# Kernel optimization log

Hardware: AMD Instinct MI355X
Metric: run time of the kernel (lower is better)

## Reference

```python
import math
import jax, jax.numpy as jnp
import numpy as np

D_MODEL = 512
H = 8          # head_num
HD = 64        # head_dim
ETA = 4
R = 8
D_FFC = 2048
EPS = 1e-6
GRU_BIAS = 2.0
T, B = 128, 32
TOTAL_PROJ = H * HD * 5 + H * ETA * 3  # 2656


def _layer_norm(x, g, b):
    m = x.mean(-1, keepdims=True)
    v = ((x - m) ** 2).mean(-1, keepdims=True)
    return (x - m) / jnp.sqrt(v + 1e-5) * g + b


def _outer(a, b):
    # a: (T,B,H,D), b: (T,B,H,E) -> (T,B,H,D*E), row-major over (D,E) like torch bmm+reshape
    t, bb, h, d = a.shape
    return (a[..., :, None] * b[..., None, :]).reshape(t, bb, h, d * b.shape[-1])


def _gru_gate(x, y, w, u):
    # GTrXL-style gating: x = residual stream, y = new signal. w,u: (3, d, d)
    r = jax.nn.sigmoid(y @ w[0].T + x @ u[0].T)
    z = jax.nn.sigmoid(y @ w[1].T + x @ u[1].T - GRU_BIAS)
    h = jnp.tanh(y @ w[2].T + (r * x) @ u[2].T)
    return (1.0 - z) * x + z * h


def _discounted_sum(prev, x, d):
    # y_t = d_t * y_{t-1} + x_t, y_{-1} = prev. x: (T, ...), d broadcastable to x.
    def step(c, xd):
        xi, di = xd
        nc = di * c + xi
        return nc, nc
    _, ys = jax.lax.scan(step, prev, (x, d))
    return ys


def setup_inputs() -> dict:
    key = jax.random.key(0)
    ks = jax.random.split(key, 12)
    sc_p = 1.0 / math.sqrt(D_MODEL)
    return {
        "inputs": jax.random.normal(ks[0], (T, B, D_MODEL), jnp.float32),
        "terminations": jax.random.randint(ks[1], (T, B), 0, 2).astype(jnp.int32),
        "tilde_k": jnp.zeros((B, R, H, ETA * HD), jnp.float32),
        "tilde_v": jnp.zeros((B, R, H, HD), jnp.float32),
        "s_prev": jnp.zeros((B, H, ETA * HD), jnp.float32),
        "tick": jnp.zeros((B, 1), jnp.float32),
        "w_proj": jax.random.normal(ks[2], (TOTAL_PROJ, D_MODEL), jnp.float32) * sc_p,
        "b_proj": jnp.zeros((TOTAL_PROJ,), jnp.float32),
        "w_attn": jax.random.normal(ks[3], (D_MODEL, H * HD), jnp.float32) * (1.0 / math.sqrt(H * HD)),
        "b_attn": jnp.zeros((D_MODEL,), jnp.float32),
        "ln1_g": jnp.ones((D_MODEL,), jnp.float32),
        "ln1_b": jnp.zeros((D_MODEL,), jnp.float32),
        "ln2_g": jnp.ones((D_MODEL,), jnp.float32),
        "ln2_b": jnp.zeros((D_MODEL,), jnp.float32),
        "gru1_w": jax.random.normal(ks[4], (3, D_MODEL, D_MODEL), jnp.float32) * sc_p,
        "gru1_u": jax.random.normal(ks[5], (3, D_MODEL, D_MODEL), jnp.float32) * sc_p,
        "gru2_w": jax.random.normal(ks[6], (3, D_MODEL, D_MODEL), jnp.float32) * sc_p,
        "gru2_u": jax.random.normal(ks[7], (3, D_MODEL, D_MODEL), jnp.float32) * sc_p,
        "ffc_w1": jax.random.normal(ks[8], (D_FFC, D_MODEL), jnp.float32) * sc_p,
        "ffc_b1": jnp.zeros((D_FFC,), jnp.float32),
        "ffc_w2": jax.random.normal(ks[9], (D_MODEL, D_FFC), jnp.float32) * (1.0 / math.sqrt(D_FFC)),
        "ffc_b2": jnp.zeros((D_MODEL,), jnp.float32),
    }


def _forward(inputs, terminations, tilde_k, tilde_v, s_prev, tick,
             w_proj, b_proj, w_attn, b_attn, ln1_g, ln1_b, ln2_g, ln2_b,
             gru1_w, gru1_u, gru2_w, gru2_u, ffc_w1, ffc_b1, ffc_w2, ffc_b2):
    t, bsz, _ = inputs.shape
    omegas = jnp.linspace(-math.pi, math.pi, R).astype(inputs.dtype)

    x_normed = _layer_norm(inputs, ln1_g, ln1_b)
    all_proj = x_normed @ w_proj.T + b_proj  # (T,B,2656)
    kqv_dim = H * HD * 5
    kqvbg = all_proj[..., :kqv_dim].reshape(t, bsz, H, 5, HD)
    p123 = all_proj[..., kqv_dim:].reshape(t, bsz, H, 3, ETA)

    keys = kqvbg[..., 0, :]
    queries = kqvbg[..., 1, :]
    values = kqvbg[..., 2, :]
    beta = jax.nn.sigmoid(kqvbg[..., 3, :])
    gammas = kqvbg[..., 4, :]
    p1, p2, p3 = p123[..., 0, :], p123[..., 1, :], p123[..., 2, :]

    keys_exp = _outer(jax.nn.relu(keys), jax.nn.relu(p1))          # (T,B,H,HD*ETA)
    queries_exp = _outer(jax.nn.relu(queries), jax.nn.relu(p2))
    gammas_exp = _outer(jax.nn.sigmoid(gammas), jax.nn.sigmoid(p3))

    ticks = tick[None] + jnp.arange(1, t + 1, dtype=tick.dtype).reshape(t, 1, 1)  # (T,B,1)
    occil = jnp.cos(ticks * omegas)  # (T,B,R)

    values_gated = values * beta                 # (T,B,H,HD)
    keys_gated = keys_exp * gammas_exp           # (T,B,H,HD*ETA)
    s_in = keys_gated
    values_osc = values_gated[:, :, None] * occil[..., None, None]  # (T,B,R,H,HD)
    keys_osc = keys_gated[:, :, None] * occil[..., None, None]      # (T,B,R,H,HD*ETA)

    term_mask = (1.0 - terminations.astype(inputs.dtype))[:, :, None, None]  # (T,B,1,1)
    discount_gamma = (1.0 - gammas_exp) * term_mask   # (T,B,H,HD*ETA)
    discount_beta = (1.0 - beta) * term_mask          # (T,B,H,HD)

    final_keys = _discounted_sum(tilde_k, keys_osc, discount_gamma[:, :, None])
    final_values = _discounted_sum(tilde_v, values_osc, discount_beta[:, :, None])
    final_s = _discounted_sum(s_prev, s_in, discount_gamma)

    kdq = (final_keys * queries_exp[:, :, None]).sum(-1)   # (T,B,R,H)
    kv = (final_values * kdq[..., None]).sum(2)             # (T,B,H,HD)
    norm = (final_s * queries_exp).sum(-1) + EPS            # (T,B,H)
    attn = kv / (2 * R * norm[..., None])
    attn = attn.reshape(t, bsz, H * HD) @ w_attn.T + b_attn  # (T,B,d_model)

    gating1 = _gru_gate(inputs, jax.nn.relu(attn), gru1_w, gru1_u)
    ffc_in = _layer_norm(gating1, ln2_g, ln2_b)
    ffc_out = jax.nn.relu(jax.nn.relu(ffc_in @ ffc_w1.T + ffc_b1) @ ffc_w2.T + ffc_b2)
    output = _gru_gate(gating1, ffc_out, gru2_w, gru2_u)
    return output


def reference(inputs, terminations, tilde_k, tilde_v, s_prev, tick,
              w_proj, b_proj, w_attn, b_attn, ln1_g, ln1_b, ln2_g, ln2_b,
              gru1_w, gru1_u, gru2_w, gru2_u, ffc_w1, ffc_b1, ffc_w2, ffc_b2):
    return _forward(inputs, terminations, tilde_k, tilde_v, s_prev, tick,
                    w_proj, b_proj, w_attn, b_attn, ln1_g, ln1_b, ln2_g, ln2_b,
                    gru1_w, gru1_u, gru2_w, gru2_u, ffc_w1, ffc_b1, ffc_w2, ffc_b2)
```

## Files before the change

kernel.cpp:

```cpp
#include <hip/hip_runtime.h>
#include <hip/hip_bf16.h>
#include <math.h>

#define DM   512
#define HH   8
#define RR   8
#define TT   128
#define BBATCH 32
#define MM   (TT*BBATCH)
#define NPROJ 2656
#define KQV  2560

typedef __attribute__((ext_vector_type(8))) short bf16x8;
typedef __attribute__((ext_vector_type(4))) float f32x4;

__device__ __forceinline__ float sigmoidf_(float x) {
    return 1.0f / (1.0f + __expf(-x));
}

__device__ __forceinline__ void gload_lds16(const void* g, void* l) {
    __builtin_amdgcn_global_load_lds(
        (const __attribute__((address_space(1))) unsigned int*)g,
        (__attribute__((address_space(3))) unsigned int*)l, 16, 0, 0);
}

template<int CTRL, int RMASK>
__device__ __forceinline__ float dpp_add_(float x) {
    union { float f; int i; } a, b;
    a.f = x;
    b.i = __builtin_amdgcn_update_dpp(0, a.i, CTRL, RMASK, 0xf, true);
    return x + b.f;
}
__device__ __forceinline__ float wave_sum_u(float x) {
    x = dpp_add_<0x111, 0xf>(x);
    x = dpp_add_<0x112, 0xf>(x);
    x = dpp_add_<0x114, 0xf>(x);
    x = dpp_add_<0x118, 0xf>(x);
    x = dpp_add_<0x142, 0xa>(x);
    x = dpp_add_<0x143, 0xc>(x);
    union { float f; int i; } s, t;
    s.f = x;
    t.i = __builtin_amdgcn_readlane(s.i, 63);
    return t.f;
}

struct F2B9 {
    const float* s[9];
    __hip_bfloat16* d[9];
    int cum[10];
};

__global__ __launch_bounds__(256) void f2b_ln_all(F2B9 a,
    const float* __restrict__ x, const float* __restrict__ g,
    const float* __restrict__ b, __hip_bfloat16* __restrict__ lnout)
{
    if (blockIdx.x < 8752) {
        int q = blockIdx.x * 256 + threadIdx.x;
        if (q >= a.cum[9]) return;
        int s = 0;
        #pragma unroll
        for (int i = 1; i < 9; ++i) s += (q >= a.cum[i]);
        int i4 = (q - a.cum[s]) * 4;
        float4 v = *(const float4*)(a.s[s] + i4);
        __hip_bfloat16* dst = a.d[s] + i4;
        dst[0] = __float2bfloat16(v.x);
        dst[1] = __float2bfloat16(v.y);
        dst[2] = __float2bfloat16(v.z);
        dst[3] = __float2bfloat16(v.w);
        return;
    }
    int row = blockIdx.x - 8752;
    int tid = threadIdx.x;
    const float* xr = x + (size_t)row * DM;
    float2 v = ((const float2*)xr)[tid];
    float s = v.x + v.y;
    #pragma unroll
    for (int off = 32; off; off >>= 1) s += __shfl_down(s, off);
    __shared__ float red[8];
    int wid = tid >> 6, lane = tid & 63;
    if (lane == 0) red[wid] = s;
    __syncthreads();
    if (tid == 0) red[0] = (red[0] + red[1] + red[2] + red[3]) * (1.0f / DM);
    __syncthreads();
    float mean = red[0];
    float dx = v.x - mean, dy = v.y - mean;
    float sq = dx*dx + dy*dy;
    #pragma unroll
    for (int off = 32; off; off >>= 1) sq += __shfl_down(sq, off);
    if (lane == 0) red[4 + wid] = sq;
    __syncthreads();
    if (tid == 0) red[1] = rsqrtf((red[4]+red[5]+red[6]+red[7]) * (1.0f/DM) + 1e-5f);
    __syncthreads();
    float rstd = red[1];
    float2 gg = ((const float2*)g)[tid];
    float2 bb = ((const float2*)b)[tid];
    __hip_bfloat16* orow = lnout + (size_t)row * DM;
    orow[2*tid+0] = __float2bfloat16(dx * rstd * gg.x + bb.x);
    orow[2*tid+1] = __float2bfloat16(dy * rstd * gg.y + bb.y);
}

__global__ __launch_bounds__(256) void ln_kernel(const float* __restrict__ x,
    const float* __restrict__ g, const float* __restrict__ b,
    __hip_bfloat16* __restrict__ out)
{
    int row = blockIdx.x;
    int tid = threadIdx.x;
    const float* xr = x + (size_t)row * DM;
    float2 v = ((const float2*)xr)[tid];
    float s = v.x + v.y;
    #pragma unroll
    for (int off = 32; off; off >>= 1) s += __shfl_down(s, off);
    __shared__ float red[8];
    int wid = tid >> 6, lane = tid & 63;
    if (lane == 0) red[wid] = s;
    __syncthreads();
    if (tid == 0) red[0] = (red[0] + red[1] + red[2] + red[3]) * (1.0f / DM);
    __syncthreads();
    float mean = red[0];
    float dx = v.x - mean, dy = v.y - mean;
    float sq = dx*dx + dy*dy;
    #pragma unroll
    for (int off = 32; off; off >>= 1) sq += __shfl_down(sq, off);
    if (lane == 0) red[4 + wid] = sq;
    __syncthreads();
    if (tid == 0) red[1] = rsqrtf((red[4]+red[5]+red[6]+red[7]) * (1.0f/DM) + 1e-5f);
    __syncthreads();
    float rstd = red[1];
    float2 gg = ((const float2*)g)[tid];
    float2 bb = ((const float2*)b)[tid];
    __hip_bfloat16* orow = out + (size_t)row * DM;
    orow[2*tid+0] = __float2bfloat16(dx * rstd * gg.x + bb.x);
    orow[2*tid+1] = __float2bfloat16(dy * rstd * gg.y + bb.y);
}

__device__ __forceinline__ void gemm_core128(
    const __hip_bfloat16* __restrict__ A, const __hip_bfloat16* __restrict__ W,
    const float* __restrict__ bias,
    float* __restrict__ Cf, __hip_bfloat16* __restrict__ Cb,
    int N, int K, int act, int m0, int n0,
    __hip_bfloat16* As, __hip_bfloat16* Bs)
{
    int tid = threadIdx.x;
    int wave = tid >> 6, lane = tid & 63;
    int wm = (wave >> 1) * 64, wn = (wave & 1) * 64;
    int fr = lane & 15, fq = lane >> 4;

    f32x4 acc[4][4];
    #pragma unroll
    for (int i = 0; i < 4; ++i)
        #pragma unroll
        for (int j = 0; j < 4; ++j)
            acc[i][j] = (f32x4){0.f, 0.f, 0.f, 0.f};

    int sm0 = wave*16 + fr;
    int sm1 = sm0 + 64;
    int wr0 = n0 + sm0; if (wr0 >= N) wr0 = N - 1;
    int wr1 = n0 + sm1; if (wr1 >= N) wr1 = N - 1;
    const __hip_bfloat16* Ag0 = A + (size_t)(m0 + sm0) * K + fq*8;
    const __hip_bfloat16* Ag1 = A + (size_t)(m0 + sm1) * K + fq*8;
    const __hip_bfloat16* Wg0 = W + (size_t)wr0 * K + fq*8;
    const __hip_bfloat16* Wg1 = W + (size_t)wr1 * K + fq*8;

    for (int k0 = 0; k0 < K; k0 += 32) {
        gload_lds16(Ag0 + k0, As + (size_t)wave*512);
        gload_lds16(Ag1 + k0, As + (size_t)(wave+4)*512);
        gload_lds16(Wg0 + k0, Bs + (size_t)wave*512);
        gload_lds16(Wg1 + k0, Bs + (size_t)(wave+4)*512);
        __syncthreads();
        bf16x8 af[4], bfr[4];
        #pragma unroll
        for (int i = 0; i < 4; ++i) {
            af[i]  = *(const bf16x8*)(As + (size_t)(wm/16 + i)*512 + lane*8);
            bfr[i] = *(const bf16x8*)(Bs + (size_t)(wn/16 + i)*512 + lane*8);
        }
        #pragma unroll
        for (int mi = 0; mi < 4; ++mi)
            #pragma unroll
            for (int ni = 0; ni < 4; ++ni)
                acc[mi][ni] = __builtin_amdgcn_mfma_f32_16x16x32_bf16(
                    af[mi], bfr[ni], acc[mi][ni], 0, 0, 0);
        __syncthreads();
    }

    #pragma unroll
    for (int ni = 0; ni < 4; ++ni) {
        int n = n0 + wn + ni*16 + fr;
        bool nok = n < N;
        float bv = (bias && nok) ? bias[n] : 0.f;
        #pragma unroll
        for (int mi = 0; mi < 4; ++mi) {
            #pragma unroll
            for (int r = 0; r < 4; ++r) {
                int m = m0 + wm + mi*16 + fq*4 + r;
                float v = acc[mi][ni][r] + bv;
                if (act) v = fmaxf(v, 0.f);
                if (nok) {
                    size_t idx = (size_t)m * N + n;
                    if (Cf) Cf[idx] = v;
                    if (Cb) Cb[idx] = __float2bfloat16(v);
                }
            }
        }
    }
}

__global__ __launch_bounds__(256) void gemm_bf16(
    const __hip_bfloat16* __restrict__ A, const __hip_bfloat16* __restrict__ W,
    const float* __restrict__ bias,
    float* __restrict__ Cf, __hip_bfloat16* __restrict__ Cb,
    int N, int K, int act)
{
    __shared__ __attribute__((aligned(16))) __hip_bfloat16 As[8*512];
    __shared__ __attribute__((aligned(16))) __hip_bfloat16 Bs[8*512];
    gemm_core128(A, W, bias, Cf, Cb, N, K, act, blockIdx.y * 128, blockIdx.x * 128, As, Bs);
}

__global__ __launch_bounds__(256) void ffc1_bx_dual(
    const __hip_bfloat16* __restrict__ Aa, const __hip_bfloat16* __restrict__ Wa,
    const float* __restrict__ biasA, __hip_bfloat16* __restrict__ CbA,
    int Na, int splitX,
    const __hip_bfloat16* __restrict__ Ab, const __hip_bfloat16* __restrict__ Wb,
    float* __restrict__ CfB, int Nb, int K)
{
    __shared__ __attribute__((aligned(16))) __hip_bfloat16 As[8*512];
    __shared__ __attribute__((aligned(16))) __hip_bfloat16 Bs[8*512];
    int bx = blockIdx.x;
    if (bx < splitX)
        gemm_core128(Aa, Wa, biasA, nullptr, CbA, Na, K, 1, blockIdx.y*128, bx*128, As, Bs);
    else
        gemm_core128(Ab, Wb, nullptr, CfB, nullptr, Nb, K, 0, blockIdx.y*128, (bx-splitX)*128, As, Bs);
}

__global__ __launch_bounds__(256) void gemm_bf16_64(
    const __hip_bfloat16* __restrict__ A, const __hip_bfloat16* __restrict__ W,
    const float* __restrict__ bias,
    float* __restrict__ Cf, __hip_bfloat16* __restrict__ Cb,
    int N, int K, int act)
{
    __shared__ __attribute__((aligned(16))) __hip_bfloat16 As[4*512];
    __shared__ __attribute__((aligned(16))) __hip_bfloat16 Bs[8*512];
    int tid = threadIdx.x;
    int wave = tid >> 6, lane = tid & 63;
    int m0 = blockIdx.y * 64, n0 = blockIdx.x * 128;
    int wm = (wave >> 1) * 32, wn = (wave & 1) * 64;
    int fr = lane & 15, fq = lane >> 4;

    f32x4 acc[2][4];
    #pragma unroll
    for (int i = 0; i < 2; ++i)
        #pragma unroll
        for (int j = 0; j < 4; ++j)
            acc[i][j] = (f32x4){0.f, 0.f, 0.f, 0.f};

    const __hip_bfloat16* Ag = A + (size_t)(m0 + wave*16 + fr) * K + fq*8;
    int wr0 = n0 + wave*16 + fr; if (wr0 >= N) wr0 = N - 1;
    int wr1 = wr0 + 64;          if (wr1 >= N) wr1 = N - 1;
    const __hip_bfloat16* Wg0 = W + (size_t)wr0 * K + fq*8;
    const __hip_bfloat16* Wg1 = W + (size_t)wr1 * K + fq*8;

    for (int k0 = 0; k0 < K; k0 += 32) {
        gload_lds16(Ag  + k0, As + (size_t)wave*512);
        gload_lds16(Wg0 + k0, Bs + (size_t)wave*512);
        gload_lds16(Wg1 + k0, Bs + (size_t)(wave+4)*512);
        __syncthreads();
        bf16x8 af[2], bfr[4];
        #pragma unroll
        for (int i = 0; i < 2; ++i)
            af[i]  = *(const bf16x8*)(As + (size_t)(wm/16 + i)*512 + lane*8);
        #pragma unroll
        for (int j = 0; j < 4; ++j)
            bfr[j] = *(const bf16x8*)(Bs + (size_t)(wn/16 + j)*512 + lane*8);
        #pragma unroll
        for (int mi = 0; mi < 2; ++mi)
            #pragma unroll
            for (int ni = 0; ni < 4; ++ni)
                acc[mi][ni] = __builtin_amdgcn_mfma_f32_16x16x32_bf16(
                    af[mi], bfr[ni], acc[mi][ni], 0, 0, 0);
        __syncthreads();
    }

    #pragma unroll
    for (int ni = 0; ni < 4; ++ni) {
        int n = n0 + wn + ni*16 + fr;
        bool nok = n < N;
        float bv = (bias && nok) ? bias[n] : 0.f;
        #pragma unroll
        for (int mi = 0; mi < 2; ++mi) {
            #pragma unroll
            for (int r = 0; r < 4; ++r) {
                int m = m0 + wm + mi*16 + fq*4 + r;
                float v = acc[mi][ni][r] + bv;
                if (act) v = fmaxf(v, 0.f);
                if (nok) {
                    size_t idx = (size_t)m * N + n;
                    if (Cf) Cf[idx] = v;
                    if (Cb) Cb[idx] = __float2bfloat16(v);
                }
            }
        }
    }
}

#define NSLOT 16
#define SLOTF 912
#define RSLOT 8
#define RSLOTF 336

__global__ __launch_bounds__(256) void scan_attn_fused(
    const float* __restrict__ proj, const int* __restrict__ term,
    const float* __restrict__ tick, const float* __restrict__ tilde_k,
    const float* __restrict__ tilde_v, const float* __restrict__ s_prev,
    __hip_bfloat16* __restrict__ attn,
    const __hip_bfloat16* __restrict__ gA, const __hip_bfloat16* __restrict__ gW,
    float* __restrict__ gC)
{
    extern __shared__ __attribute__((aligned(16))) char smem_dyn[];
    int bid = blockIdx.x;
    if (bid >= 256) {
        __hip_bfloat16* As = (__hip_bfloat16*)smem_dyn;
        __hip_bfloat16* Bs = As + 8*512;
        int g = bid - 256;
        gemm_core128(gA, gW, nullptr, gC, nullptr, 1024, DM, 0,
                     (g >> 3) * 128, (g & 7) * 128, As, Bs);
        return;
    }

    float* slots    = (float*)smem_dyn;
    float* raw      = slots + NSLOT*SLOTF;
    int*   raw_flag = (int*)(raw + RSLOT*RSLOTF);
    int*   ctrs     = raw_flag + 32;

    const int b = bid >> 3;
    const int h = bid & 7;
    const int tid = threadIdx.x;
    const int wv = tid >> 6, lane = tid & 63;

    if (tid == 0) { ctrs[0] = 0; ctrs[1] = 0; }
    if (tid < 32) raw_flag[tid] = 0;
    __syncthreads();
    int* prod_ctr = &ctrs[0];
    int* cons_ctr = &ctrs[1];

    const float PI_ = 3.14159265358979323846f;

    if (wv >= 2) {
        for (int g = wv - 2; g < TT/4; g += 2) {
            int t0 = g * 4;
            if (t0 >= RSLOT) {
                while (__hip_atomic_load(prod_ctr, __ATOMIC_ACQUIRE,
                                         __HIP_MEMORY_SCOPE_WORKGROUP) < t0 - 4)
                    __builtin_amdgcn_s_sleep(1);
            }
            float va[4][5]; float pv[4];
            #pragma unroll
            for (int i = 0; i < 4; ++i) {
                const float* prow = proj + (size_t)((t0+i)*BBATCH + b) * NPROJ;
                const float* p5 = prow + h*320;
                va[i][0] = p5[lane];
                va[i][1] = p5[64  + lane];
                va[i][2] = p5[128 + lane];
                va[i][3] = p5[192 + lane];
                va[i][4] = p5[256 + lane];
                pv[i] = (lane < 12) ? prow[KQV + h*12 + lane] : 0.f;
            }
            #pragma unroll
            for (int i = 0; i < 4; ++i) {
                float* rs = raw + (size_t)((t0+i) & (RSLOT-1)) * RSLOTF;
                rs[lane]       = va[i][0];
                rs[64  + lane] = va[i][1];
                rs[128 + lane] = va[i][2];
                rs[192 + lane] = va[i][3];
                rs[256 + lane] = va[i][4];
                if (lane < 12) rs[320 + lane] = pv[i];
            }
            if (lane == 0)
                __hip_atomic_store(&raw_flag[g], 1, __ATOMIC_RELEASE,
                                   __HIP_MEMORY_SCOPE_WORKGROUP);
        }
        return;
    }

    if (wv == 1) {
        float tk = tick[b];
        int ta  = term[lane*BBATCH + b];
        int tb_ = term[(64 + lane)*BBATCH + b];
        float wv_ = -PI_ + (float)(lane & 7) * (2.0f * PI_ / 7.0f);
        float cwv = cosf(wv_), swv = sinf(wv_);
        float ocv = cosf((tk + 1.0f) * wv_), osv = sinf((tk + 1.0f) * wv_);

        for (int t0 = 0; t0 < TT; t0 += 4) {
            if (t0 >= NSLOT) {
                while (__hip_atomic_load(cons_ctr, __ATOMIC_ACQUIRE,
                                         __HIP_MEMORY_SCOPE_WORKGROUP) < t0 - (NSLOT - 4))
                    __builtin_amdgcn_s_sleep(1);
            }
            int g = t0 >> 2;
            while (__hip_atomic_load(&raw_flag[g], __ATOMIC_ACQUIRE,
                                     __HIP_MEMORY_SCOPE_WORKGROUP) == 0)
                __builtin_amdgcn_s_sleep(1);
            float va[4][5]; float4 P1[4], P2[4], P3[4];
            #pragma unroll
            for (int i = 0; i < 4; ++i) {
                const float* rs = raw + (size_t)((t0+i) & (RSLOT-1)) * RSLOTF;
                va[i][0] = rs[lane];
                va[i][1] = rs[64  + lane];
                va[i][2] = rs[128 + lane];
                va[i][3] = rs[192 + lane];
                va[i][4] = rs[256 + lane];
                P1[i] = *(const float4*)(rs + 320);
                P2[i] = *(const float4*)(rs + 324);
                P3[i] = *(const float4*)(rs + 328);
            }
            #pragma unroll
            for (int i = 0; i < 4; ++i) {
                int t = t0 + i;
                int tm = (t < 64) ? __builtin_amdgcn_readlane(ta, t)
                                  : __builtin_amdgcn_readlane(tb_, t - 64);
                float mask = 1.0f - (float)tm;
                float kr = fmaxf(va[i][0], 0.f);
                float qr = fmaxf(va[i][1], 0.f);
                float sg = sigmoidf_(va[i][4]);
                float sb = sigmoidf_(va[i][3]);
                float vg = va[i][2] * sb;
                float db = (1.f - sb) * mask;
                float p1a[4] = {P1[i].x, P1[i].y, P1[i].z, P1[i].w};
                float p2a[4] = {P2[i].x, P2[i].y, P2[i].z, P2[i].w};
                float p3a[4] = {P3[i].x, P3[i].y, P3[i].z, P3[i].w};
                float4 qe, kgv, dgv;
                #pragma unroll
                for (int j = 0; j < 4; ++j) {
                    float kexp = kr * fmaxf(p1a[j], 0.f);
                    float qq   = qr * fmaxf(p2a[j], 0.f);
                    float gexp = sg * sigmoidf_(p3a[j]);
                    float kg_  = kexp * gexp;
                    float dg_  = (1.f - gexp) * mask;
                    if (j == 0) { qe.x = qq; kgv.x = kg_; dgv.x = dg_; }
                    if (j == 1) { qe.y = qq; kgv.y = kg_; dgv.y = dg_; }
                    if (j == 2) { qe.z = qq; kgv.z = kg_; dgv.z = dg_; }
                    if (j == 3) { qe.w = qq; kgv.w = kg_; dgv.w = dg_; }
                }
                float* sl = slots + (size_t)(t & (NSLOT-1)) * SLOTF;
                *(float4*)(sl + 4*lane)       = qe;
                *(float4*)(sl + 256 + 4*lane) = kgv;
                *(float4*)(sl + 512 + 4*lane) = dgv;
                sl[768 + lane] = vg;
                sl[832 + lane] = db;
                if (lane < 8) sl[896 + lane] = ocv;
                float cc = ocv, ss = osv;
                ocv = cc*cwv - ss*swv;
                osv = ss*cwv + cc*swv;
            }
            if (lane == 0)
                __hip_atomic_store(prod_ctr, t0 + 4, __ATOMIC_RELEASE,
                                   __HIP_MEMORY_SCOPE_WORKGROUP);
        }
        return;
    }

    float4 fs = *(const float4*)(s_prev + ((size_t)(b*HH + h))*256 + lane*4);
    float4 fk[8];
    #pragma unroll
    for (int r = 0; r < 8; ++r)
        fk[r] = *(const float4*)(tilde_k + (((size_t)b*RR + r)*HH + h)*256 + lane*4);
    float fv[8];
    #pragma unroll
    for (int r = 0; r < 8; ++r)
        fv[r] = tilde_v[(((size_t)b*RR + r)*HH + h)*64 + lane];

    struct PF { float4 qe, kg, dg, o0, o1; float vg, db; };
    auto loadPF = [&](int t, PF& p) {
        if (t < TT) {
            const float* sl = slots + (size_t)(t & (NSLOT-1)) * SLOTF;
            p.qe = *(const float4*)(sl + 4*lane);
            p.kg = *(const float4*)(sl + 256 + 4*lane);
            p.dg = *(const float4*)(sl + 512 + 4*lane);
            p.vg = sl[768 + lane];
            p.db = sl[832 + lane];
            p.o0 = *(const float4*)(sl + 896);
            p.o1 = *(const float4*)(sl + 900);
        }
    };

    auto step = [&](int t, PF c) {
        float qexp[4] = {c.qe.x, c.qe.y, c.qe.z, c.qe.w};
        float kg[4]   = {c.kg.x, c.kg.y, c.kg.z, c.kg.w};
        float dg[4]   = {c.dg.x, c.dg.y, c.dg.z, c.dg.w};
        float occ[8]  = {c.o0.x, c.o0.y, c.o0.z, c.o0.w,
                         c.o1.x, c.o1.y, c.o1.z, c.o1.w};
        fs.x = dg[0]*fs.x + kg[0];
        fs.y = dg[1]*fs.y + kg[1];
        fs.z = dg[2]*fs.z + kg[2];
        fs.w = dg[3]*fs.w + kg[3];
        float snorm = fs.x*qexp[0] + fs.y*qexp[1] + fs.z*qexp[2] + fs.w*qexp[3];
        float kdq[8];
        #pragma unroll
        for (int r = 0; r < 8; ++r) {
            float4 f = fk[r];
            float o = occ[r];
            f.x = dg[0]*f.x + kg[0]*o;
            f.y = dg[1]*f.y + kg[1]*o;
            f.z = dg[2]*f.z + kg[2]*o;
            f.w = dg[3]*f.w + kg[3]*o;
            fk[r] = f;
            kdq[r] = f.x*qexp[0] + f.y*qexp[1] + f.z*qexp[2] + f.w*qexp[3];
        }
        #pragma unroll
        for (int r = 0; r < 8; ++r)
            fv[r] = c.db * fv[r] + c.vg * occ[r];
        float nrm_u = wave_sum_u(snorm);
        float kdq_u[8];
        #pragma unroll
        for (int r = 0; r < 8; ++r)
            kdq_u[r] = wave_sum_u(kdq[r]);
        float kv = 0.f;
        #pragma unroll
        for (int r = 0; r < 8; ++r)
            kv += fv[r] * kdq_u[r];
        attn[(size_t)(t*BBATCH + b)*DM + h*64 + lane] =
            __float2bfloat16(kv / (16.f * (nrm_u + 1e-6f)));
    };

    while (__hip_atomic_load(prod_ctr, __ATOMIC_ACQUIRE,
                             __HIP_MEMORY_SCOPE_WORKGROUP) < 8)
        __builtin_amdgcn_s_sleep(1);
    PF pf0, pf1;
    loadPF(0, pf0);
    loadPF(1, pf1);

    for (int t = 0; t < TT; t += 2) {
        if ((t & 3) == 0) {
            if ((t & 7) == 0 && t >= 8 && lane == 0)
                __hip_atomic_store(cons_ctr, t - 2, __ATOMIC_RELEASE,
                                   __HIP_MEMORY_SCOPE_WORKGROUP);
            int tgt = (t + 8 > TT) ? TT : t + 8;
            while (__hip_atomic_load(prod_ctr, __ATOMIC_ACQUIRE,
                                     __HIP_MEMORY_SCOPE_WORKGROUP) < tgt)
                __builtin_amdgcn_s_sleep(1);
        }
        PF c0 = pf0; loadPF(t + 2, pf0);
        step(t, c0);
        PF c1 = pf1; loadPF(t + 3, pf1);
        step(t + 1, c1);
    }
}

__global__ __launch_bounds__(256) void gru_rz_kernel(const float* __restrict__ A1,
    const float* __restrict__ Bx, const float* __restrict__ x,
    __hip_bfloat16* __restrict__ rx, float* __restrict__ z)
{
    size_t i = (size_t)blockIdx.x * 256 + threadIdx.x;
    size_t m = i >> 9;
    int c = (int)(i & 511);
    float rpre = A1[m*1536 + c]       + Bx[m*1024 + c];
    float zpre = A1[m*1536 + 512 + c] + Bx[m*1024 + 512 + c] - 2.0f;
    rx[i] = __float2bfloat16(sigmoidf_(rpre) * x[i]);
    z[i]  = sigmoidf_(zpre);
}

__global__ __launch_bounds__(256) void gru_final_kernel(const float* __restrict__ A1,
    const float* __restrict__ C2, const float* __restrict__ z,
    const float* __restrict__ x, float* __restrict__ out)
{
    size_t i = (size_t)blockIdx.x * 256 + threadIdx.x;
    size_t m = i >> 9;
    int c = (int)(i & 511);
    float hh = tanhf(A1[m*1536 + 1024 + c] + C2[i]);
    float zz = z[i];
    out[i] = (1.0f - zz) * x[i] + zz * hh;
}

__global__ __launch_bounds__(256) void gru_final_ln(
    const float* __restrict__ A1, const float* __restrict__ C2,
    const float* __restrict__ z, const float* __restrict__ x,
    const float* __restrict__ g, const float* __restrict__ bta,
    float* __restrict__ g1, __hip_bfloat16* __restrict__ g1b,
    __hip_bfloat16* __restrict__ fib)
{
    int row = blockIdx.x;
    int tid = threadIdx.x;
    size_t base = (size_t)row * DM;
    float2 c2v = ((const float2*)(C2 + base))[tid];
    float2 zv  = ((const float2*)(z  + base))[tid];
    float2 xv  = ((const float2*)(x  + base))[tid];
    float2 av  = ((const float2*)(A1 + (size_t)row*1536 + 1024))[tid];
    float h0 = tanhf(av.x + c2v.x);
    float h1 = tanhf(av.y + c2v.y);
    float2 v;
    v.x = (1.0f - zv.x) * xv.x + zv.x * h0;
    v.y = (1.0f - zv.y) * xv.y + zv.y * h1;
    ((float2*)(g1 + base))[tid] = v;
    g1b[base + 2*tid+0] = __float2bfloat16(v.x);
    g1b[base + 2*tid+1] = __float2bfloat16(v.y);

    float s = v.x + v.y;
    #pragma unroll
    for (int off = 32; off; off >>= 1) s += __shfl_down(s, off);
    __shared__ float red[8];
    int wid = tid >> 6, lane = tid & 63;
    if (lane == 0) red[wid] = s;
    __syncthreads();
    if (tid == 0) red[0] = (red[0] + red[1] + red[2] + red[3]) * (1.0f / DM);
    __syncthreads();
    float mean = red[0];
    float dx = v.x - mean, dy = v.y - mean;
    float sq = dx*dx + dy*dy;
    #pragma unroll
    for (int off = 32; off; off >>= 1) sq += __shfl_down(sq, off);
    if (lane == 0) red[4 + wid] = sq;
    __syncthreads();
    if (tid == 0) red[1] = rsqrtf((red[4]+red[5]+red[6]+red[7]) * (1.0f/DM) + 1e-5f);
    __syncthreads();
    float rstd = red[1];
    float2 gg = ((const float2*)g)[tid];
    float2 bb = ((const float2*)bta)[tid];
    fib[base + 2*tid+0] = __float2bfloat16(dx * rstd * gg.x + bb.x);
    fib[base + 2*tid+1] = __float2bfloat16(dy * rstd * gg.y + bb.y);
}

extern "C" void kernel_launch(void* const* d_in, const int* in_sizes, int n_in,
                              void* d_out, int out_size, void* d_ws, size_t ws_size,
                              hipStream_t stream)
{
    const float* inputs = (const float*)d_in[0];
    const int*   term   = (const int*)  d_in[1];
    const float* tilde_k= (const float*)d_in[2];
    const float* tilde_v= (const float*)d_in[3];
    const float* s_prev = (const float*)d_in[4];
    const float* tick   = (const float*)d_in[5];
    const float* w_proj = (const float*)d_in[6];
    const float* b_proj = (const float*)d_in[7];
    const float* w_attn = (const float*)d_in[8];
    const float* b_attn = (const float*)d_in[9];
    const float* ln1_g  = (const float*)d_in[10];
    const float* ln1_b  = (const float*)d_in[11];
    const float* ln2_g  = (const float*)d_in[12];
    const float* ln2_b  = (const float*)d_in[13];
    const float* gru1_w = (const float*)d_in[14];
    const float* gru1_u = (const float*)d_in[15];
    const float* gru2_w = (const float*)d_in[16];
    const float* gru2_u = (const float*)d_in[17];
    const float* ffc_w1 = (const float*)d_in[18];
    const float* ffc_b1 = (const float*)d_in[19];
    const float* ffc_w2 = (const float*)d_in[20];
    const float* ffc_b2 = (const float*)d_in[21];
    float* out = (float*)d_out;
    float* ws  = (float*)d_ws;

    float* proj = ws;
    float* A1   = ws;
    float* C2   = ws + 10878976;
    float* zb   = ws + 12976128;
    float* g1   = ws + 15073280;
    __hip_bfloat16* bb = (__hip_bfloat16*)(ws + 17170432);
    __hip_bfloat16* wp_bf  = bb + 0;
    __hip_bfloat16* wat_bf = bb + 1359872;
    __hip_bfloat16* g1w_bf = bb + 1622016;
    __hip_bfloat16* g1u_bf = bb + 2408448;
    __hip_bfloat16* g2w_bf = bb + 3194880;
    __hip_bfloat16* g2u_bf = bb + 3981312;
    __hip_bfloat16* fw1_bf = bb + 4767744;
    __hip_bfloat16* fw2_bf = bb + 5816320;
    __hip_bfloat16* in_bf  = bb + 6864896;
    __hip_bfloat16* xn_bf  = bb + 8962048;
    __hip_bfloat16* at_bf  = bb + 11059200;
    __hip_bfloat16* y1_bf  = bb + 13156352;
    __hip_bfloat16* rx_bf  = bb + 15253504;
    __hip_bfloat16* fi_bf  = bb + 17350656;
    __hip_bfloat16* mid_bf = bb + 19447808;
    __hip_bfloat16* fo_bf  = bb + 27836416;
    __hip_bfloat16* g1_bf  = bb + 29933568;
    float* Bx = ws + 33185792;

    dim3 blk(256);

    F2B9 fa;
    const float* srcs[9] = {w_proj, w_attn, gru1_w, gru1_u, gru2_w, gru2_u,
                            ffc_w1, ffc_w2, inputs};
    __hip_bfloat16* dsts[9] = {wp_bf, wat_bf, g1w_bf, g1u_bf, g2w_bf, g2u_bf,
                               fw1_bf, fw2_bf, in_bf};
    int quads[9] = {339968, 65536, 196608, 196608, 196608, 196608,
                    262144, 262144, 524288};
    int cum = 0;
    for (int i = 0; i < 9; ++i) { fa.s[i] = srcs[i]; fa.d[i] = dsts[i]; fa.cum[i] = cum; cum += quads[i]; }
    fa.cum[9] = cum;
    f2b_ln_all<<<8752 + MM, blk, 0, stream>>>(fa, inputs, ln1_g, ln1_b, xn_bf);

    gemm_bf16<<<dim3(21, 32), blk, 0, stream>>>(xn_bf, wp_bf, b_proj, proj, nullptr, NPROJ, DM, 0);

    size_t dyn = (size_t)(NSLOT*SLOTF + RSLOT*RSLOTF + 64) * 4;
    scan_attn_fused<<<512, blk, dyn, stream>>>(proj, term, tick, tilde_k, tilde_v,
                                               s_prev, at_bf, in_bf, g1u_bf, Bx);

    gemm_bf16_64<<<dim3(4, 64), blk, 0, stream>>>(at_bf, wat_bf, b_attn, nullptr, y1_bf, DM, DM, 1);

    gemm_bf16<<<dim3(12, 32), blk, 0, stream>>>(y1_bf, g1w_bf, nullptr, A1, nullptr, 3*DM, DM, 0);
    gru_rz_kernel<<<MM*DM/256, blk, 0, stream>>>(A1, Bx, inputs, rx_bf, zb);
    gemm_bf16_64<<<dim3(4, 64), blk, 0, stream>>>(rx_bf, g1u_bf + 2*DM*DM, nullptr, C2, nullptr, DM, DM, 0);
    gru_final_ln<<<MM, blk, 0, stream>>>(A1, C2, zb, inputs, ln2_g, ln2_b, g1, g1_bf, fi_bf);

    ffc1_bx_dual<<<dim3(24, 32), blk, 0, stream>>>(fi_bf, fw1_bf, ffc_b1, mid_bf,
                                                   2048, 16,
                                                   g1_bf, g2u_bf, Bx, 1024, DM);

    gemm_bf16_64<<<dim3(4, 64), blk, 0, stream>>>(mid_bf, fw2_bf, ffc_b2, nullptr, fo_bf, DM, 2048, 1);

    gemm_bf16<<<dim3(12, 32), blk, 0, stream>>>(fo_bf, g2w_bf, nullptr, A1, nullptr, 3*DM, DM, 0);
    gru_rz_kernel<<<MM*DM/256, blk, 0, stream>>>(A1, Bx, g1, rx_bf, zb);
    gemm_bf16_64<<<dim3(4, 64), blk, 0, stream>>>(rx_bf, g2u_bf + 2*DM*DM, nullptr, C2, nullptr, DM, DM, 0);
    gru_final_kernel<<<MM*DM/256, blk, 0, stream>>>(A1, C2, zb, g1, out);
}
```

Before: 478.2 us.

## Replace producer-consumer scan pipeline with chunked parallel scan across four waves

The recurrent scan over 128 timesteps is split into four 32-step chunks, one per wave. Waves first sweep their chunk from zero state while accumulating decay products, then pass carried state to the next wave through LDS boundary buffers and combine it. A second sweep with the corrected initial state emits the attention outputs. This replaces the old single-consumer design, which had loader and gate-precompute waves feeding one scanning wave, and cuts the serial chain length in exchange for roughly twice the scan arithmetic and a serial boundary handoff. It also removes the unused ln_kernel and precomputes the oscillator cosines into a table.

```diff
diff --git a/kernel.cpp b/kernel.cpp
--- a/kernel.cpp
+++ b/kernel.cpp
@@ -99,40 +99,6 @@
     orow[2*tid+1] = __float2bfloat16(dy * rstd * gg.y + bb.y);
 }
 
-__global__ __launch_bounds__(256) void ln_kernel(const float* __restrict__ x,
-    const float* __restrict__ g, const float* __restrict__ b,
-    __hip_bfloat16* __restrict__ out)
-{
-    int row = blockIdx.x;
-    int tid = threadIdx.x;
-    const float* xr = x + (size_t)row * DM;
-    float2 v = ((const float2*)xr)[tid];
-    float s = v.x + v.y;
-    #pragma unroll
-    for (int off = 32; off; off >>= 1) s += __shfl_down(s, off);
-    __shared__ float red[8];
-    int wid = tid >> 6, lane = tid & 63;
-    if (lane == 0) red[wid] = s;
-    __syncthreads();
-    if (tid == 0) red[0] = (red[0] + red[1] + red[2] + red[3]) * (1.0f / DM);
-    __syncthreads();
-    float mean = red[0];
-    float dx = v.x - mean, dy = v.y - mean;
-    float sq = dx*dx + dy*dy;
-    #pragma unroll
-    for (int off = 32; off; off >>= 1) sq += __shfl_down(sq, off);
-    if (lane == 0) red[4 + wid] = sq;
-    __syncthreads();
-    if (tid == 0) red[1] = rsqrtf((red[4]+red[5]+red[6]+red[7]) * (1.0f/DM) + 1e-5f);
-    __syncthreads();
-    float rstd = red[1];
-    float2 gg = ((const float2*)g)[tid];
-    float2 bb = ((const float2*)b)[tid];
-    __hip_bfloat16* orow = out + (size_t)row * DM;
-    orow[2*tid+0] = __float2bfloat16(dx * rstd * gg.x + bb.x);
-    orow[2*tid+1] = __float2bfloat16(dy * rstd * gg.y + bb.y);
-}
-
 __device__ __forceinline__ void gemm_core128(
     const __hip_bfloat16* __restrict__ A, const __hip_bfloat16* __restrict__ W,
     const float* __restrict__ bias,
@@ -301,10 +267,9 @@
     }
 }
 
-#define NSLOT 16
-#define SLOTF 912
-#define RSLOT 8
-#define RSLOTF 336
+#define NCH   4
+#define CHK   32
+#define BNDF  (44*64)
 
 __global__ __launch_bounds__(256) void scan_attn_fused(
     const float* __restrict__ proj, const int* __restrict__ term,
@@ -325,223 +290,195 @@
         return;
     }
 
-    float* slots    = (float*)smem_dyn;
-    float* raw      = slots + NSLOT*SLOTF;
-    int*   raw_flag = (int*)(raw + RSLOT*RSLOTF);
-    int*   ctrs     = raw_flag + 32;
-
-    const int b = bid >> 3;
-    const int h = bid & 7;
+    float* bnd  = (float*)smem_dyn;
+    float* occt = bnd + 3*BNDF;
+    int*   flags= (int*)(occt + TT*8);
+
+    const int b = bid >> 3, h = bid & 7;
     const int tid = threadIdx.x;
     const int wv = tid >> 6, lane = tid & 63;
-
-    if (tid == 0) { ctrs[0] = 0; ctrs[1] = 0; }
-    if (tid < 32) raw_flag[tid] = 0;
-    __syncthreads();
-    int* prod_ctr = &ctrs[0];
-    int* cons_ctr = &ctrs[1];
-
-    const float PI_ = 3.14159265358979323846f;
-
-    if (wv >= 2) {
-        for (int g = wv - 2; g < TT/4; g += 2) {
-            int t0 = g * 4;
-            if (t0 >= RSLOT) {
-                while (__hip_atomic_load(prod_ctr, __ATOMIC_ACQUIRE,
-                                         __HIP_MEMORY_SCOPE_WORKGROUP) < t0 - 4)
-                    __builtin_amdgcn_s_sleep(1);
+    const int t0 = wv * CHK;
+
+    const float tk = tick[b];
+    if (tid < 4) flags[tid] = 0;
+    {
+        const float PI_ = 3.14159265358979323846f;
+        #pragma unroll
+        for (int i = 0; i < 4; ++i) {
+            int idx = tid*4 + i;
+            int t = idx >> 3, r = idx & 7;
+            float w = -PI_ + (float)r * (2.0f*PI_/7.0f);
+            occt[idx] = cosf((tk + (float)(t + 1)) * w);
+        }
+    }
+    __syncthreads();
+
+    int tmv = (lane < CHK) ? term[(size_t)(t0 + lane)*BBATCH + b] : 0;
+
+    float fs[4], fk[8][4], fv[8], Pg[4], Pb;
+
+    auto zero_state = [&]() {
+        #pragma unroll
+        for (int j = 0; j < 4; ++j) fs[j] = 0.f;
+        #pragma unroll
+        for (int r = 0; r < 8; ++r) {
+            #pragma unroll
+            for (int j = 0; j < 4; ++j) fk[r][j] = 0.f;
+            fv[r] = 0.f;
+        }
+    };
+    auto load_init = [&]() {
+        float4 s4 = *(const float4*)(s_prev + ((size_t)(b*HH + h))*256 + lane*4);
+        fs[0]=s4.x; fs[1]=s4.y; fs[2]=s4.z; fs[3]=s4.w;
+        #pragma unroll
+        for (int r = 0; r < 8; ++r) {
+            float4 k4 = *(const float4*)(tilde_k + (((size_t)b*RR + r)*HH + h)*256 + lane*4);
+            fk[r][0]=k4.x; fk[r][1]=k4.y; fk[r][2]=k4.z; fk[r][3]=k4.w;
+            fv[r] = tilde_v[(((size_t)b*RR + r)*HH + h)*64 + lane];
+        }
+    };
+    auto load_bnd = [&](int w) {
+        const float* p = bnd + w*BNDF;
+        #pragma unroll
+        for (int j = 0; j < 4; ++j) fs[j] = p[j*64 + lane];
+        #pragma unroll
+        for (int r = 0; r < 8; ++r) {
+            #pragma unroll
+            for (int j = 0; j < 4; ++j) fk[r][j] = p[(4 + r*4 + j)*64 + lane];
+            fv[r] = p[(36 + r)*64 + lane];
+        }
+    };
+    auto store_bnd = [&](int w) {
+        float* p = bnd + w*BNDF;
+        #pragma unroll
+        for (int j = 0; j < 4; ++j) p[j*64 + lane] = fs[j];
+        #pragma unroll
+        for (int r = 0; r < 8; ++r) {
+            #pragma unroll
+            for (int j = 0; j < 4; ++j) p[(4 + r*4 + j)*64 + lane] = fk[r][j];
+            p[(36 + r)*64 + lane] = fv[r];
+        }
+    };
+    auto combine = [&](int w) {
+        const float* p = bnd + w*BNDF;
+        #pragma unroll
+        for (int j = 0; j < 4; ++j) fs[j] = fmaf(Pg[j], p[j*64 + lane], fs[j]);
+        #pragma unroll
+        for (int r = 0; r < 8; ++r) {
+            #pragma unroll
+            for (int j = 0; j < 4; ++j)
+                fk[r][j] = fmaf(Pg[j], p[(4 + r*4 + j)*64 + lane], fk[r][j]);
+            fv[r] = fmaf(Pb, p[(36 + r)*64 + lane], fv[r]);
+        }
+    };
+
+    struct Raw { float k, q, v, be, ga; float4 P1, P2, P3; };
+    auto load_raw = [&](int t, Raw& rw) {
+        const float* prow = proj + (size_t)(t*BBATCH + b) * NPROJ;
+        const float* p5 = prow + h*320;
+        rw.k  = p5[lane];
+        rw.q  = p5[64  + lane];
+        rw.v  = p5[128 + lane];
+        rw.be = p5[192 + lane];
+        rw.ga = p5[256 + lane];
+        const float* pp = prow + KQV + h*12;
+        rw.P1 = *(const float4*)(pp);
+        rw.P2 = *(const float4*)(pp + 4);
+        rw.P3 = *(const float4*)(pp + 8);
+    };
+
+    auto sweep = [&](bool out) {
+        Pg[0]=Pg[1]=Pg[2]=Pg[3]=1.f; Pb=1.f;
+        Raw cur, nxt;
+        load_raw(t0, cur);
+        for (int i = 0; i < CHK; ++i) {
+            const int t = t0 + i;
+            if (i + 1 < CHK) load_raw(t + 1, nxt);
+            const int tm = __builtin_amdgcn_readlane(tmv, i);
+            const float mask = 1.0f - (float)tm;
+            float kr = fmaxf(cur.k, 0.f);
+            float sg = sigmoidf_(cur.ga);
+            float sb = sigmoidf_(cur.be);
+            float vg = cur.v * sb;
+            float db = (1.f - sb) * mask;
+            float p1a[4] = {cur.P1.x, cur.P1.y, cur.P1.z, cur.P1.w};
+            float p3a[4] = {cur.P3.x, cur.P3.y, cur.P3.z, cur.P3.w};
+            float kg[4], dg[4];
+            #pragma unroll
+            for (int j = 0; j < 4; ++j) {
+                float gexp = sg * sigmoidf_(p3a[j]);
+                kg[j] = kr * fmaxf(p1a[j], 0.f) * gexp;
+                dg[j] = (1.f - gexp) * mask;
             }
-            float va[4][5]; float pv[4];
-            #pragma unroll
-            for (int i = 0; i < 4; ++i) {
-                const float* prow = proj + (size_t)((t0+i)*BBATCH + b) * NPROJ;
-                const float* p5 = prow + h*320;
-                va[i][0] = p5[lane];
-                va[i][1] = p5[64  + lane];
-                va[i][2] = p5[128 + lane];
-                va[i][3] = p5[192 + lane];
-                va[i][4] = p5[256 + lane];
-                pv[i] = (lane < 12) ? prow[KQV + h*12 + lane] : 0.f;
+            float occ[8];
+            {
+                float4 o0 = *(const float4*)(occt + t*8);
+                float4 o1 = *(const float4*)(occt + t*8 + 4);
+                occ[0]=o0.x; occ[1]=o0.y; occ[2]=o0.z; occ[3]=o0.w;
+                occ[4]=o1.x; occ[5]=o1.y; occ[6]=o1.z; occ[7]=o1.w;
             }
             #pragma unroll
-            for (int i = 0; i < 4; ++i) {
-                float* rs = raw + (size_t)((t0+i) & (RSLOT-1)) * RSLOTF;
-                rs[lane]       = va[i][0];
-                rs[64  + lane] = va[i][1];
-                rs[128 + lane] = va[i][2];
-                rs[192 + lane] = va[i][3];
-                rs[256 + lane] = va[i][4];
-                if (lane < 12) rs[320 + lane] = pv[i];
+            for (int j = 0; j < 4; ++j) {
+                fs[j] = fmaf(dg[j], fs[j], kg[j]);
+                Pg[j] *= dg[j];
             }
-            if (lane == 0)
-                __hip_atomic_store(&raw_flag[g], 1, __ATOMIC_RELEASE,
-                                   __HIP_MEMORY_SCOPE_WORKGROUP);
-        }
-        return;
-    }
-
-    if (wv == 1) {
-        float tk = tick[b];
-        int ta  = term[lane*BBATCH + b];
-        int tb_ = term[(64 + lane)*BBATCH + b];
-        float wv_ = -PI_ + (float)(lane & 7) * (2.0f * PI_ / 7.0f);
-        float cwv = cosf(wv_), swv = sinf(wv_);
-        float ocv = cosf((tk + 1.0f) * wv_), osv = sinf((tk + 1.0f) * wv_);
-
-        for (int t0 = 0; t0 < TT; t0 += 4) {
-            if (t0 >= NSLOT) {
-                while (__hip_atomic_load(cons_ctr, __ATOMIC_ACQUIRE,
-                                         __HIP_MEMORY_SCOPE_WORKGROUP) < t0 - (NSLOT - 4))
-                    __builtin_amdgcn_s_sleep(1);
+            #pragma unroll
+            for (int r = 0; r < 8; ++r) {
+                #pragma unroll
+                for (int j = 0; j < 4; ++j)
+                    fk[r][j] = fmaf(dg[j], fk[r][j], kg[j]*occ[r]);
+                fv[r] = fmaf(db, fv[r], vg*occ[r]);
             }
-            int g = t0 >> 2;
-            while (__hip_atomic_load(&raw_flag[g], __ATOMIC_ACQUIRE,
+            Pb *= db;
+            if (out) {
+                float qr = fmaxf(cur.q, 0.f);
+                float p2a[4] = {cur.P2.x, cur.P2.y, cur.P2.z, cur.P2.w};
+                float qe[4];
+                #pragma unroll
+                for (int j = 0; j < 4; ++j) qe[j] = qr * fmaxf(p2a[j], 0.f);
+                float snorm = fs[0]*qe[0] + fs[1]*qe[1] + fs[2]*qe[2] + fs[3]*qe[3];
+                float nrm_u = wave_sum_u(snorm);
+                float kdq_u[8];
+                #pragma unroll
+                for (int r = 0; r < 8; ++r) {
+                    float kdq = fk[r][0]*qe[0] + fk[r][1]*qe[1]
+                              + fk[r][2]*qe[2] + fk[r][3]*qe[3];
+                    kdq_u[r] = wave_sum_u(kdq);
+                }
+                float kv = 0.f;
+                #pragma unroll
+                for (int r = 0; r < 8; ++r) kv = fmaf(fv[r], kdq_u[r], kv);
+                attn[(size_t)(t*BBATCH + b)*DM + h*64 + lane] =
+                    __float2bfloat16(kv / (16.f * (nrm_u + 1e-6f)));
+            }
+            cur = nxt;
+        }
+    };
+
+    if (wv < NCH - 1) {
+        if (wv == 0) load_init(); else zero_state();
+        sweep(false);
+        if (wv > 0) {
+            while (__hip_atomic_load(&flags[wv-1], __ATOMIC_ACQUIRE,
                                      __HIP_MEMORY_SCOPE_WORKGROUP) == 0)
                 __builtin_amdgcn_s_sleep(1);
-            float va[4][5]; float4 P1[4], P2[4], P3[4];
-            #pragma unroll
-            for (int i = 0; i < 4; ++i) {
-                const float* rs = raw + (size_t)((t0+i) & (RSLOT-1)) * RSLOTF;
-                va[i][0] = rs[lane];
-                va[i][1] = rs[64  + lane];
-                va[i][2] = rs[128 + lane];
-                va[i][3] = rs[192 + lane];
-                va[i][4] = rs[256 + lane];
-                P1[i] = *(const float4*)(rs + 320);
-                P2[i] = *(const float4*)(rs + 324);
-                P3[i] = *(const float4*)(rs + 328);
-            }
-            #pragma unroll
-            for (int i = 0; i < 4; ++i) {
-                int t = t0 + i;
-                int tm = (t < 64) ? __builtin_amdgcn_readlane(ta, t)
-                                  : __builtin_amdgcn_readlane(tb_, t - 64);
-                float mask = 1.0f - (float)tm;
-                float kr = fmaxf(va[i][0], 0.f);
-                float qr = fmaxf(va[i][1], 0.f);
-                float sg = sigmoidf_(va[i][4]);
-                float sb = sigmoidf_(va[i][3]);
-                float vg = va[i][2] * sb;
-                float db = (1.f - sb) * mask;
-                float p1a[4] = {P1[i].x, P1[i].y, P1[i].z, P1[i].w};
-                float p2a[4] = {P2[i].x, P2[i].y, P2[i].z, P2[i].w};
-                float p3a[4] = {P3[i].x, P3[i].y, P3[i].z, P3[i].w};
-                float4 qe, kgv, dgv;
-                #pragma unroll
-                for (int j = 0; j < 4; ++j) {
-                    float kexp = kr * fmaxf(p1a[j], 0.f);
-                    float qq   = qr * fmaxf(p2a[j], 0.f);
-                    float gexp = sg * sigmoidf_(p3a[j]);
-                    float kg_  = kexp * gexp;
-                    float dg_  = (1.f - gexp) * mask;
-                    if (j == 0) { qe.x = qq; kgv.x = kg_; dgv.x = dg_; }
-                    if (j == 1) { qe.y = qq; kgv.y = kg_; dgv.y = dg_; }
-                    if (j == 2) { qe.z = qq; kgv.z = kg_; dgv.z = dg_; }
-                    if (j == 3) { qe.w = qq; kgv.w = kg_; dgv.w = dg_; }
-                }
-                float* sl = slots + (size_t)(t & (NSLOT-1)) * SLOTF;
-                *(float4*)(sl + 4*lane)       = qe;
-                *(float4*)(sl + 256 + 4*lane) = kgv;
-                *(float4*)(sl + 512 + 4*lane) = dgv;
-                sl[768 + lane] = vg;
-                sl[832 + lane] = db;
-                if (lane < 8) sl[896 + lane] = ocv;
-                float cc = ocv, ss = osv;
-                ocv = cc*cwv - ss*swv;
-                osv = ss*cwv + cc*swv;
-            }
-            if (lane == 0)
-                __hip_atomic_store(prod_ctr, t0 + 4, __ATOMIC_RELEASE,
-                                   __HIP_MEMORY_SCOPE_WORKGROUP);
-        }
-        return;
-    }
-
-    float4 fs = *(const float4*)(s_prev + ((size_t)(b*HH + h))*256 + lane*4);
-    float4 fk[8];
-    #pragma unroll
-    for (int r = 0; r < 8; ++r)
-        fk[r] = *(const float4*)(tilde_k + (((size_t)b*RR + r)*HH + h)*256 + lane*4);
-    float fv[8];
-    #pragma unroll
-    for (int r = 0; r < 8; ++r)
-        fv[r] = tilde_v[(((size_t)b*RR + r)*HH + h)*64 + lane];
-
-    struct PF { float4 qe, kg, dg, o0, o1; float vg, db; };
-    auto loadPF = [&](int t, PF& p) {
-        if (t < TT) {
-            const float* sl = slots + (size_t)(t & (NSLOT-1)) * SLOTF;
-            p.qe = *(const float4*)(sl + 4*lane);
-            p.kg = *(const float4*)(sl + 256 + 4*lane);
-            p.dg = *(const float4*)(sl + 512 + 4*lane);
-            p.vg = sl[768 + lane];
-            p.db = sl[832 + lane];
-            p.o0 = *(const float4*)(sl + 896);
-            p.o1 = *(const float4*)(sl + 900);
-        }
-    };
-
-    auto step = [&](int t, PF c) {
-        float qexp[4] = {c.qe.x, c.qe.y, c.qe.z, c.qe.w};
-        float kg[4]   = {c.kg.x, c.kg.y, c.kg.z, c.kg.w};
-        float dg[4]   = {c.dg.x, c.dg.y, c.dg.z, c.dg.w};
-        float occ[8]  = {c.o0.x, c.o0.y, c.o0.z, c.o0.w,
-                         c.o1.x, c.o1.y, c.o1.z, c.o1.w};
-        fs.x = dg[0]*fs.x + kg[0];
-        fs.y = dg[1]*fs.y + kg[1];
-        fs.z = dg[2]*fs.z + kg[2];
-        fs.w = dg[3]*fs.w + kg[3];
-        float snorm = fs.x*qexp[0] + fs.y*qexp[1] + fs.z*qexp[2] + fs.w*qexp[3];
-        float kdq[8];
-        #pragma unroll
-        for (int r = 0; r < 8; ++r) {
-            float4 f = fk[r];
-            float o = occ[r];
-            f.x = dg[0]*f.x + kg[0]*o;
-            f.y = dg[1]*f.y + kg[1]*o;
-            f.z = dg[2]*f.z + kg[2]*o;
-            f.w = dg[3]*f.w + kg[3]*o;
-            fk[r] = f;
-            kdq[r] = f.x*qexp[0] + f.y*qexp[1] + f.z*qexp[2] + f.w*qexp[3];
-        }
-        #pragma unroll
-        for (int r = 0; r < 8; ++r)
-            fv[r] = c.db * fv[r] + c.vg * occ[r];
-        float nrm_u = wave_sum_u(snorm);
-        float kdq_u[8];
-        #pragma unroll
-        for (int r = 0; r < 8; ++r)
-            kdq_u[r] = wave_sum_u(kdq[r]);
-        float kv = 0.f;
-        #pragma unroll
-        for (int r = 0; r < 8; ++r)
-            kv += fv[r] * kdq_u[r];
-        attn[(size_t)(t*BBATCH + b)*DM + h*64 + lane] =
-            __float2bfloat16(kv / (16.f * (nrm_u + 1e-6f)));
-    };
-
-    while (__hip_atomic_load(prod_ctr, __ATOMIC_ACQUIRE,
-                             __HIP_MEMORY_SCOPE_WORKGROUP) < 8)
-        __builtin_amdgcn_s_sleep(1);
-    PF pf0, pf1;
-    loadPF(0, pf0);
-    loadPF(1, pf1);
-
-    for (int t = 0; t < TT; t += 2) {
-        if ((t & 3) == 0) {
-            if ((t & 7) == 0 && t >= 8 && lane == 0)
-                __hip_atomic_store(cons_ctr, t - 2, __ATOMIC_RELEASE,
-                                   __HIP_MEMORY_SCOPE_WORKGROUP);
-            int tgt = (t + 8 > TT) ? TT : t + 8;
-            while (__hip_atomic_load(prod_ctr, __ATOMIC_ACQUIRE,
-                                     __HIP_MEMORY_SCOPE_WORKGROUP) < tgt)
-                __builtin_amdgcn_s_sleep(1);
-        }
-        PF c0 = pf0; loadPF(t + 2, pf0);
-        step(t, c0);
-        PF c1 = pf1; loadPF(t + 3, pf1);
-        step(t + 1, c1);
-    }
+            combine(wv - 1);
+        }
+        store_bnd(wv);
+        if (lane == 0)
+            __hip_atomic_store(&flags[wv], 1, __ATOMIC_RELEASE,
+                               __HIP_MEMORY_SCOPE_WORKGROUP);
+    }
+
+    if (wv == 0) {
+        load_init();
+    } else {
+        while (__hip_atomic_load(&flags[wv-1], __ATOMIC_ACQUIRE,
+                                 __HIP_MEMORY_SCOPE_WORKGROUP) == 0)
+            __builtin_amdgcn_s_sleep(1);
+        load_bnd(wv - 1);
+    }
+    sweep(true);
 }
 
 __global__ __launch_bounds__(256) void gru_rz_kernel(const float* __restrict__ A1,
@@ -687,7 +624,7 @@
 
     gemm_bf16<<<dim3(21, 32), blk, 0, stream>>>(xn_bf, wp_bf, b_proj, proj, nullptr, NPROJ, DM, 0);
 
-    size_t dyn = (size_t)(NSLOT*SLOTF + RSLOT*RSLOTF + 64) * 4;
+    size_t dyn = (size_t)(3*BNDF + TT*8 + 4) * 4;
     scan_attn_fused<<<512, blk, dyn, stream>>>(proj, term, tick, tilde_k, tilde_v,
                                                s_prev, at_bf, in_bf, g1u_bf, Bx);
 
```

Result: faster. 408.6 us (-14.5%).
